# Optimization experiments

Hardware: AMD Instinct MI355X
Metric: run time of the kernel (lower is better)

## Reference

```python
import jax, jax.numpy as jnp
import numpy as np

BETA = 0.25  # commitment loss weight


def setup_inputs() -> dict:
    key = jax.random.key(0)
    ks = jax.random.split(key, 6)
    B, H, W, C = 16, 64, 64, 128
    x = jax.random.normal(ks[0], (B, H, W, C), dtype=jnp.float32)
    # dictionaries: sizes 2^6 .. 2^9 (from num_embeddings=[64,512]),
    # keras RandomUniform default init in (-0.05, 0.05)
    dicts = {}
    for i, n_emb in enumerate([64, 128, 256, 512]):
        dicts[f"dict{i}"] = jax.random.uniform(
            ks[i + 1], (C, n_emb), dtype=jnp.float32, minval=-0.05, maxval=0.05)
    vq_alpha = jnp.asarray(1.0, dtype=jnp.float32)
    vq_gamma = jnp.full((4,), 0.25, dtype=jnp.float32)  # 1/num_dictionaries
    return {"x": x, **dicts, "vq_alpha": vq_alpha, "vq_gamma": vq_gamma}


def _vq_pass(flat, D):
    # flat: [N, C], D: [C, K]. Squared-euclidean distances then argmin.
    dist = (jnp.sum(flat * flat, axis=1, keepdims=True)
            + jnp.sum(D * D, axis=0)[None, :]
            - 2.0 * (flat @ D))  # [N, K]
    idx = jnp.argmin(dist, axis=1)  # [N]
    # one_hot @ D.T  ==  gather rows of D.T
    return jnp.take(D.T, idx, axis=0)  # [N, C]


def reference(x, dict0, dict1, dict2, dict3, vq_alpha, vq_gamma):
    dicts = [dict0, dict1, dict2, dict3]
    C = x.shape[-1]
    flat = x.reshape(-1, C)  # [N, C]
    weighted_q = jnp.zeros_like(x)
    dictionary_loss = jnp.asarray(0.0, x.dtype)
    commitment_loss = jnp.asarray(0.0, x.dtype)
    for i, D in enumerate(dicts):
        q = (vq_alpha * _vq_pass(flat, D)).reshape(x.shape)
        weighted_q = weighted_q + vq_gamma[i] * q
        dictionary_loss += vq_gamma[i] * jnp.mean(
            jnp.square(jax.lax.stop_gradient(x) - q))
        commitment_loss += vq_gamma[i] * jnp.mean(
            jnp.square(x - jax.lax.stop_gradient(q)))
    loss = dictionary_loss + BETA * commitment_loss
    # straight-through estimator
    out = x + jax.lax.stop_gradient(weighted_q - x)
    return out, loss
```

## Files before the change

kernel.cpp:

```cpp
#include <hip/hip_runtime.h>

#define CDIM 128
#define NC   8388608

typedef __attribute__((ext_vector_type(8)))  short bf8v;
typedef __attribute__((ext_vector_type(16))) float f32x16;


__device__ __forceinline__ void bsplit(float v, short& h, short& lo) {
  unsigned u = __float_as_uint(v);
  unsigned hb = (u + 0x7fffu + ((u >> 16) & 1u)) >> 16;
  float hf = __uint_as_float(hb << 16);
  float lf = v - hf;
  unsigned u2 = __float_as_uint(lf);
  unsigned lb = (u2 + 0x7fffu + ((u2 >> 16) & 1u)) >> 16;
  h = (short)hb; lo = (short)lb;
}

__global__ void vq_prep(const float* __restrict__ D0, const float* __restrict__ D1,
                        const float* __restrict__ D2, const float* __restrict__ D3,
                        float* __restrict__ nrm, float* __restrict__ DT,
                        bf8v* __restrict__ Bph, bf8v* __restrict__ Bpl) {
  const int b = blockIdx.x;
  if (b < 60) {
    int g = b * 256 + threadIdx.x;
    int T = g >> 9, c = (g >> 6) & 7, l = g & 63;
    int col = T * 32 + (l & 31);
    int k0 = c * 16 + (l >> 5) * 8;
    const float* D; int K, cb;
    if (col < 64)       { D = D0; K = 64;  cb = col; }
    else if (col < 192) { D = D1; K = 128; cb = col - 64; }
    else if (col < 448) { D = D2; K = 256; cb = col - 192; }
    else                { D = D3; K = 512; cb = col - 448; }
    short h0,h1,h2,h3,h4,h5,h6,h7, q0,q1,q2,q3,q4,q5,q6,q7;
    bsplit(D[(k0+0)*K + cb], h0, q0);
    bsplit(D[(k0+1)*K + cb], h1, q1);
    bsplit(D[(k0+2)*K + cb], h2, q2);
    bsplit(D[(k0+3)*K + cb], h3, q3);
    bsplit(D[(k0+4)*K + cb], h4, q4);
    bsplit(D[(k0+5)*K + cb], h5, q5);
    bsplit(D[(k0+6)*K + cb], h6, q6);
    bsplit(D[(k0+7)*K + cb], h7, q7);
    Bph[g] = (bf8v){h0,h1,h2,h3,h4,h5,h6,h7};
    Bpl[g] = (bf8v){q0,q1,q2,q3,q4,q5,q6,q7};
  } else {
    int g = (b - 60) * 256 + threadIdx.x;
    if (g >= 960) return;
    const float* D; int K, k; float* T;
    if (g < 64)       { D = D0; K = 64;  k = g;       T = DT; }
    else if (g < 192) { D = D1; K = 128; k = g - 64;  T = DT + 8192; }
    else if (g < 448) { D = D2; K = 256; k = g - 192; T = DT + 24576; }
    else              { D = D3; K = 512; k = g - 448; T = DT + 57344; }
    float s = 0.f;
    for (int c = 0; c < 128; ++c) { float v = D[c*K+k]; s = fmaf(v,v,s); T[k*128+c] = v; }
    nrm[g] = s;
  }
}

#define MK8(U0, U1, HD, LD) { \
  short h0,h1,h2,h3,h4,h5,h6,h7, q0,q1,q2,q3,q4,q5,q6,q7; \
  bsplit(U0.x,h0,q0); bsplit(U0.y,h1,q1); bsplit(U0.z,h2,q2); bsplit(U0.w,h3,q3); \
  bsplit(U1.x,h4,q4); bsplit(U1.y,h5,q5); bsplit(U1.z,h6,q6); bsplit(U1.w,h7,q7); \
  HD = (bf8v){h0,h1,h2,h3,h4,h5,h6,h7}; \
  LD = (bf8v){q0,q1,q2,q3,q4,q5,q6,q7}; }

#define MFMA32(AC, AF, BF) AC = __builtin_amdgcn_mfma_f32_32x32x16_bf16((AF), (BF), (AC), 0, 0, 0)

#define PF_T(TT) { \
  const bf8v* __restrict__ gh = Bph + (TT) * 512; \
  const bf8v* __restrict__ gl = Bpl + (TT) * 512; \
  pf0 = gh[t]; pf1 = gh[256 + t]; pf2 = gl[t]; pf3 = gl[256 + t]; }

#define STORE_T(BF) { \
  BL[BF][t] = pf0; BL[BF][256 + t] = pf1; BL[BF][512 + t] = pf2; BL[BF][768 + t] = pf3; }

#define COMPUTE_T(T, BF) { \
  f32x16 ae = zero16, ao = zero16; \
  _Pragma("unroll") \
  for (int cp = 0; cp < 4; ++cp) { \
    const int ce = 2*cp, co = 2*cp+1; \
    bf8v bhe = BL[BF][ce*64 + l]; bf8v bho = BL[BF][co*64 + l]; \
    bf8v ble = BL[BF][512 + ce*64 + l]; bf8v blo = BL[BF][512 + co*64 + l]; \
    MFMA32(ae, Ah[ce], bhe); MFMA32(ao, Ah[co], bho); \
    MFMA32(ae, Al[ce], bhe); MFMA32(ao, Al[co], bho); \
    MFMA32(ae, Ah[ce], ble); MFMA32(ao, Ah[co], blo); \
  } \
  f32x16 sv = ae + ao; \
  const float nv = nrm_g[(T)*32 + (l & 31)]; \
  const int colT = (T)*32 + (l & 31); \
  _Pragma("unroll") \
  for (int r = 0; r < 16; ++r) { \
    float c0 = fmaf(-2.f, sv[r], nv); \
    if (c0 < bc[r]) { bc[r] = c0; bk[r] = colT; } } }

#define ROUND_T(T) { \
  if ((T) < 29) { \
    STORE_T(((T) + 1) & 1); \
    const int TN = ((T) + 2 <= 29) ? (T) + 2 : 29; \
    PF_T(TN); \
  } \
  COMPUTE_T(T, (T) & 1) \
  __syncthreads(); }

#define FLUSH1(DICTID, BASE, GAM) { \
  _Pragma("unroll") \
  for (int r = 0; r < 16; ++r) { \
    float b0 = bc[r]; int K0 = bk[r]; \
    _Pragma("unroll") \
    for (int m = 1; m <= 16; m <<= 1) { \
      float pb = __shfl_xor(b0, m); int pk = __shfl_xor(K0, m); \
      if (pb < b0 || (pb == b0 && pk < K0)) { b0 = pb; K0 = pk; } } \
    if ((l & 31) == 0) { \
      const int ro = (r & 3) + 8 * (r >> 2) + 4 * hl; \
      keysL[DICTID][w * 32 + ro] = K0 - (BASE); \
      const float nst = nrm_g[K0]; \
       \
      lossacc = fmaf((GAM) * a, fmaf(am1, nst, b0), lossacc); } \
    bc[r] = 1e30f; bk[r] = 0; } }

__global__ __launch_bounds__(256, 2) void vq_mfma(
    const float* __restrict__ x,
    const bf8v* __restrict__ Bph, const bf8v* __restrict__ Bpl,
    const float* __restrict__ nrm_g, const float* __restrict__ DT,
    const float* __restrict__ alpha_p, const float* __restrict__ gamma_p,
    float* __restrict__ out, float* __restrict__ partials)
{
  __shared__ bf8v  BL[2][1024];
  __shared__ int   keysL[4][128];
  __shared__ float lossW[4];

  const int t = threadIdx.x;
  const int w = t >> 6, l = t & 63;
  const int hl = l >> 5;
  const int rowbase = blockIdx.x * 128 + w * 32;

  const float a  = alpha_p[0];
  const float am1 = a - 1.f;
  const float g0 = gamma_p[0], g1 = gamma_p[1], g2 = gamma_p[2], g3 = gamma_p[3];
  const float gsum = g0 + g1 + g2 + g3;

  bf8v Ah[8], Al[8];
  float xsqh = 0.f;
  {
    const float* __restrict__ xr = x + (size_t)(rowbase + (l & 31)) * CDIM + hl * 8;
    #pragma unroll
    for (int c = 0; c < 8; ++c) {
      float4 u0 = *(const float4*)(xr + c * 16);
      float4 u1 = *(const float4*)(xr + c * 16 + 4);
      xsqh = fmaf(u0.x,u0.x, xsqh); xsqh = fmaf(u0.y,u0.y, xsqh);
      xsqh = fmaf(u0.z,u0.z, xsqh); xsqh = fmaf(u0.w,u0.w, xsqh);
      xsqh = fmaf(u1.x,u1.x, xsqh); xsqh = fmaf(u1.y,u1.y, xsqh);
      xsqh = fmaf(u1.z,u1.z, xsqh); xsqh = fmaf(u1.w,u1.w, xsqh);
      MK8(u0, u1, Ah[c], Al[c])
    }
  }
  float xs_ = xsqh;
  #pragma unroll
  for (int m = 1; m <= 32; m <<= 1) xs_ += __shfl_xor(xs_, m);

  f32x16 zero16;
  #pragma unroll
  for (int i = 0; i < 16; ++i) zero16[i] = 0.f;

  float bc[16]; int bk[16];
  #pragma unroll
  for (int r = 0; r < 16; ++r) { bc[r] = 1e30f; bk[r] = 0; }
  float lossacc = 0.f;

  bf8v pf0, pf1, pf2, pf3;
  PF_T(0)
  STORE_T(0)
  PF_T(1)
  __syncthreads();

  ROUND_T(0) ROUND_T(1)
  FLUSH1(0, 0, g0)
  for (int T = 2; T < 6; ++T) ROUND_T(T)
  FLUSH1(1, 64, g1)
  for (int T = 6; T < 14; ++T) ROUND_T(T)
  FLUSH1(2, 192, g2)
  for (int T = 14; T < 30; ++T) ROUND_T(T)
  FLUSH1(3, 448, g3)

  {
    float wl = lossacc + __shfl_xor(lossacc, 32);
    if (l == 0) lossW[w] = fmaf(gsum, xs_, wl);
  }
  __syncthreads();
  if (t == 0) partials[blockIdx.x] = lossW[0] + lossW[1] + lossW[2] + lossW[3];

  #pragma unroll 4
  for (int j = 0; j < 16; ++j) {
    const int f = j * 256 + t;
    const int r = f >> 5, c4 = (f & 31) * 4;
    const int kk0 = keysL[0][r], kk1 = keysL[1][r];
    const int kk2 = keysL[2][r], kk3 = keysL[3][r];
    const size_t off = (size_t)(blockIdx.x * 128 + r) * CDIM + c4;
    const float4 d0 = *(const float4*)(DT +         kk0 * 128 + c4);
    const float4 d1 = *(const float4*)(DT +  8192 + kk1 * 128 + c4);
    const float4 d2 = *(const float4*)(DT + 24576 + kk2 * 128 + c4);
    const float4 d3 = *(const float4*)(DT + 57344 + kk3 * 128 + c4);
    float4 o;
    o.x = a * (g0*d0.x + g1*d1.x + g2*d2.x + g3*d3.x);
    o.y = a * (g0*d0.y + g1*d1.y + g2*d2.y + g3*d3.y);
    o.z = a * (g0*d0.z + g1*d1.z + g2*d2.z + g3*d3.z);
    o.w = a * (g0*d0.w + g1*d1.w + g2*d2.w + g3*d3.w);
    *(float4*)(out + off) = o;
  }
}

__global__ void vq_loss(const float* __restrict__ partials, float* __restrict__ lossp) {
  __shared__ float wr[4];
  const int t = threadIdx.x;
  float v = partials[t] + partials[t + 256];
  #pragma unroll
  for (int off = 32; off > 0; off >>= 1) v += __shfl_down(v, off);
  if ((t & 63) == 0) wr[t >> 6] = v;
  __syncthreads();
  if (t == 0) lossp[0] = (wr[0] + wr[1] + wr[2] + wr[3]) * (1.25f / 8388608.f);
}

extern "C" void kernel_launch(void* const* d_in, const int* in_sizes, int n_in,
                              void* d_out, int out_size, void* d_ws, size_t ws_size,
                              hipStream_t stream) {
  const float* x  = (const float*)d_in[0];
  const float* D0 = (const float*)d_in[1];
  const float* D1 = (const float*)d_in[2];
  const float* D2 = (const float*)d_in[3];
  const float* D3 = (const float*)d_in[4];
  const float* alpha = (const float*)d_in[5];
  const float* gamma = (const float*)d_in[6];
  float* out = (float*)d_out;

  float* ws  = (float*)d_ws;
  float* nrm = ws;
  float* DT  = ws + 1024;
  bf8v*  Bph = (bf8v*)(ws + 123904);
  bf8v*  Bpl = (bf8v*)(ws + 185344);
  float* partials = ws + 246784;

  vq_prep<<<64, 256, 0, stream>>>(D0, D1, D2, D3, nrm, DT, Bph, Bpl);
  vq_mfma<<<512, 256, 0, stream>>>(x, Bph, Bpl, nrm, DT, alpha, gamma, out, partials);
  vq_loss<<<1, 256, 0, stream>>>(partials, out + NC);
}
```

Before: 104.2 us.

## Split codebook tiles across wave pairs and move gather-output into separate kernel

Each block now handles 64 rows instead of 128. Two waves scan dictionaries 0-2 (14 tiles) while the other two scan dictionary 3 (16 tiles) in parallel on the same rows, which halves the serial tile chain per wave. The grid doubles to 1024 blocks and occupancy is raised to 4 blocks per CU. Argmin keys go to a global buffer, and a new vq_merge kernel gathers and writes the weighted output. In exchange there is an extra launch and a key round-trip through memory, the prefetch-through-registers pipelining is replaced by synchronous staging with two barriers per round, and the part-0 waves sit idle for the last two rounds.

```diff
diff --git a/kernel.cpp b/kernel.cpp
--- a/kernel.cpp
+++ b/kernel.cpp
@@ -66,43 +66,38 @@
 
 #define MFMA32(AC, AF, BF) AC = __builtin_amdgcn_mfma_f32_32x32x16_bf16((AF), (BF), (AC), 0, 0, 0)
 
-#define PF_T(TT) { \
-  const bf8v* __restrict__ gh = Bph + (TT) * 512; \
-  const bf8v* __restrict__ gl = Bpl + (TT) * 512; \
-  pf0 = gh[t]; pf1 = gh[256 + t]; pf2 = gl[t]; pf3 = gl[256 + t]; }
-
-#define STORE_T(BF) { \
-  BL[BF][t] = pf0; BL[BF][256 + t] = pf1; BL[BF][512 + t] = pf2; BL[BF][768 + t] = pf3; }
-
-#define COMPUTE_T(T, BF) { \
+#define STAGE17(TP0, TP1, DO0) { \
+  if (DO0) { \
+    BL[0][t]       = Bph[(TP0) * 512 + t]; \
+    BL[0][256 + t] = Bph[(TP0) * 512 + 256 + t]; \
+    BL[0][512 + t] = Bpl[(TP0) * 512 + t]; \
+    BL[0][768 + t] = Bpl[(TP0) * 512 + 256 + t]; \
+  } \
+  BL[1][t]       = Bph[(TP1) * 512 + t]; \
+  BL[1][256 + t] = Bph[(TP1) * 512 + 256 + t]; \
+  BL[1][512 + t] = Bpl[(TP1) * 512 + t]; \
+  BL[1][768 + t] = Bpl[(TP1) * 512 + 256 + t]; }
+
+#define COMPUTE17(TT) { \
   f32x16 ae = zero16, ao = zero16; \
   _Pragma("unroll") \
   for (int cp = 0; cp < 4; ++cp) { \
     const int ce = 2*cp, co = 2*cp+1; \
-    bf8v bhe = BL[BF][ce*64 + l]; bf8v bho = BL[BF][co*64 + l]; \
-    bf8v ble = BL[BF][512 + ce*64 + l]; bf8v blo = BL[BF][512 + co*64 + l]; \
+    bf8v bhe = BL[part][ce*64 + l]; bf8v bho = BL[part][co*64 + l]; \
+    bf8v ble = BL[part][512 + ce*64 + l]; bf8v blo = BL[part][512 + co*64 + l]; \
     MFMA32(ae, Ah[ce], bhe); MFMA32(ao, Ah[co], bho); \
     MFMA32(ae, Al[ce], bhe); MFMA32(ao, Al[co], bho); \
     MFMA32(ae, Ah[ce], ble); MFMA32(ao, Ah[co], blo); \
   } \
   f32x16 sv = ae + ao; \
-  const float nv = nrm_g[(T)*32 + (l & 31)]; \
-  const int colT = (T)*32 + (l & 31); \
+  const float nv = nrm_g[(TT)*32 + (l & 31)]; \
+  const int colT = (TT)*32 + (l & 31); \
   _Pragma("unroll") \
   for (int r = 0; r < 16; ++r) { \
     float c0 = fmaf(-2.f, sv[r], nv); \
     if (c0 < bc[r]) { bc[r] = c0; bk[r] = colT; } } }
 
-#define ROUND_T(T) { \
-  if ((T) < 29) { \
-    STORE_T(((T) + 1) & 1); \
-    const int TN = ((T) + 2 <= 29) ? (T) + 2 : 29; \
-    PF_T(TN); \
-  } \
-  COMPUTE_T(T, (T) & 1) \
-  __syncthreads(); }
-
-#define FLUSH1(DICTID, BASE, GAM) { \
+#define FLUSH17(DICTID, BASE, GAM) { \
   _Pragma("unroll") \
   for (int r = 0; r < 16; ++r) { \
     float b0 = bc[r]; int K0 = bk[r]; \
@@ -112,29 +107,29 @@
       if (pb < b0 || (pb == b0 && pk < K0)) { b0 = pb; K0 = pk; } } \
     if ((l & 31) == 0) { \
       const int ro = (r & 3) + 8 * (r >> 2) + 4 * hl; \
-      keysL[DICTID][w * 32 + ro] = K0 - (BASE); \
+      keys[((rowbase + ro) << 2) | (DICTID)] = K0 - (BASE); \
       const float nst = nrm_g[K0]; \
-       \
       lossacc = fmaf((GAM) * a, fmaf(am1, nst, b0), lossacc); } \
     bc[r] = 1e30f; bk[r] = 0; } }
 
-__global__ __launch_bounds__(256, 2) void vq_mfma(
+__global__ __launch_bounds__(256, 4) void vq_mfma(
     const float* __restrict__ x,
     const bf8v* __restrict__ Bph, const bf8v* __restrict__ Bpl,
-    const float* __restrict__ nrm_g, const float* __restrict__ DT,
+    const float* __restrict__ nrm_g,
     const float* __restrict__ alpha_p, const float* __restrict__ gamma_p,
-    float* __restrict__ out, float* __restrict__ partials)
+    int* __restrict__ keys, float* __restrict__ partials)
 {
   __shared__ bf8v  BL[2][1024];
-  __shared__ int   keysL[4][128];
   __shared__ float lossW[4];
 
   const int t = threadIdx.x;
   const int w = t >> 6, l = t & 63;
   const int hl = l >> 5;
-  const int rowbase = blockIdx.x * 128 + w * 32;
-
-  const float a  = alpha_p[0];
+  const int rowt = w & 1;
+  const int part = w >> 1;
+  const int rowbase = blockIdx.x * 64 + rowt * 32;
+
+  const float a   = alpha_p[0];
   const float am1 = a - 1.f;
   const float g0 = gamma_p[0], g1 = gamma_p[1], g2 = gamma_p[2], g3 = gamma_p[3];
   const float gsum = g0 + g1 + g2 + g3;
@@ -167,39 +162,55 @@
   for (int r = 0; r < 16; ++r) { bc[r] = 1e30f; bk[r] = 0; }
   float lossacc = 0.f;
 
-  bf8v pf0, pf1, pf2, pf3;
-  PF_T(0)
-  STORE_T(0)
-  PF_T(1)
-  __syncthreads();
-
-  ROUND_T(0) ROUND_T(1)
-  FLUSH1(0, 0, g0)
-  for (int T = 2; T < 6; ++T) ROUND_T(T)
-  FLUSH1(1, 64, g1)
-  for (int T = 6; T < 14; ++T) ROUND_T(T)
-  FLUSH1(2, 192, g2)
-  for (int T = 14; T < 30; ++T) ROUND_T(T)
-  FLUSH1(3, 448, g3)
+  STAGE17(0, 14, true)
+  __syncthreads();
+
+  #pragma unroll 1
+  for (int r16i = 0; r16i < 16; ++r16i) {
+    if (part == 1) { COMPUTE17(14 + r16i) }
+    else if (r16i < 14) { COMPUTE17(r16i) }
+    if (part == 0) {
+      if (r16i == 1)       FLUSH17(0,   0, g0)
+      else if (r16i == 5)  FLUSH17(1,  64, g1)
+      else if (r16i == 13) FLUSH17(2, 192, g2)
+    } else if (r16i == 15) FLUSH17(3, 448, g3)
+    __syncthreads();
+    if (r16i < 15) {
+      const int n0 = (r16i + 1 < 14) ? r16i + 1 : 13;
+      STAGE17(n0, 15 + r16i, (r16i + 1 < 14))
+      __syncthreads();
+    }
+  }
 
   {
     float wl = lossacc + __shfl_xor(lossacc, 32);
-    if (l == 0) lossW[w] = fmaf(gsum, xs_, wl);
+    if (l == 0) lossW[w] = (part == 0) ? fmaf(gsum, xs_, wl) : wl;
   }
   __syncthreads();
   if (t == 0) partials[blockIdx.x] = lossW[0] + lossW[1] + lossW[2] + lossW[3];
-
-  #pragma unroll 4
-  for (int j = 0; j < 16; ++j) {
+}
+
+__global__ __launch_bounds__(256, 8) void vq_merge(
+    const float* __restrict__ DT, const int* __restrict__ keys,
+    const float* __restrict__ alpha_p, const float* __restrict__ gamma_p,
+    float* __restrict__ out)
+{
+  __shared__ int kk[32][4];
+  const int t = threadIdx.x;
+  const int row0 = blockIdx.x * 32;
+  if (t < 128) kk[t >> 2][t & 3] = keys[((row0 + (t >> 2)) << 2) | (t & 3)];
+  __syncthreads();
+  const float a = alpha_p[0];
+  const float g0 = gamma_p[0], g1 = gamma_p[1], g2 = gamma_p[2], g3 = gamma_p[3];
+  #pragma unroll
+  for (int j = 0; j < 4; ++j) {
     const int f = j * 256 + t;
     const int r = f >> 5, c4 = (f & 31) * 4;
-    const int kk0 = keysL[0][r], kk1 = keysL[1][r];
-    const int kk2 = keysL[2][r], kk3 = keysL[3][r];
-    const size_t off = (size_t)(blockIdx.x * 128 + r) * CDIM + c4;
-    const float4 d0 = *(const float4*)(DT +         kk0 * 128 + c4);
-    const float4 d1 = *(const float4*)(DT +  8192 + kk1 * 128 + c4);
-    const float4 d2 = *(const float4*)(DT + 24576 + kk2 * 128 + c4);
-    const float4 d3 = *(const float4*)(DT + 57344 + kk3 * 128 + c4);
+    const size_t off = (size_t)(row0 + r) * CDIM + c4;
+    const float4 d0 = *(const float4*)(DT +         kk[r][0] * 128 + c4);
+    const float4 d1 = *(const float4*)(DT +  8192 + kk[r][1] * 128 + c4);
+    const float4 d2 = *(const float4*)(DT + 24576 + kk[r][2] * 128 + c4);
+    const float4 d3 = *(const float4*)(DT + 57344 + kk[r][3] * 128 + c4);
     float4 o;
     o.x = a * (g0*d0.x + g1*d1.x + g2*d2.x + g3*d3.x);
     o.y = a * (g0*d0.y + g1*d1.y + g2*d2.y + g3*d3.y);
@@ -212,7 +223,7 @@
 __global__ void vq_loss(const float* __restrict__ partials, float* __restrict__ lossp) {
   __shared__ float wr[4];
   const int t = threadIdx.x;
-  float v = partials[t] + partials[t + 256];
+  float v = partials[t] + partials[t + 256] + partials[t + 512] + partials[t + 768];
   #pragma unroll
   for (int off = 32; off > 0; off >>= 1) v += __shfl_down(v, off);
   if ((t & 63) == 0) wr[t >> 6] = v;
@@ -237,9 +248,11 @@
   float* DT  = ws + 1024;
   bf8v*  Bph = (bf8v*)(ws + 123904);
   bf8v*  Bpl = (bf8v*)(ws + 185344);
-  float* partials = ws + 246784;
+  int*  keys = (int*)(ws + 246784);
+  float* partials = ws + 508928;
 
   vq_prep<<<64, 256, 0, stream>>>(D0, D1, D2, D3, nrm, DT, Bph, Bpl);
-  vq_mfma<<<512, 256, 0, stream>>>(x, Bph, Bpl, nrm, DT, alpha, gamma, out, partials);
+  vq_mfma<<<1024, 256, 0, stream>>>(x, Bph, Bpl, nrm, alpha, gamma, keys, partials);
+  vq_merge<<<2048, 256, 0, stream>>>(DT, keys, alpha, gamma, out);
   vq_loss<<<1, 256, 0, stream>>>(partials, out + NC);
 }
```

After: 204.8 us. +96.5%, slower.

## Split output gather into separate merge kernel via global key buffer

Applied to the files above, without the earlier changes.

Moves the final gather-and-weighted-sum of dictionary rows out of the MFMA distance kernel into a new vq_merge kernel with 2048 small blocks. The argmin indices are written to a global keys buffer instead of shared memory. The intent is to spread the memory-bound output write across many more blocks and free the compute kernel from the tail store phase. The cost is an extra kernel launch, a global round trip for the keys, and no overlap between the store and the MFMA work inside one block.

```diff
diff --git a/kernel.cpp b/kernel.cpp
--- a/kernel.cpp
+++ b/kernel.cpp
@@ -102,7 +102,7 @@
   COMPUTE_T(T, (T) & 1) \
   __syncthreads(); }
 
-#define FLUSH1(DICTID, BASE, GAM) { \
+#define FLUSHG(DICTID, BASE, GAM) { \
   _Pragma("unroll") \
   for (int r = 0; r < 16; ++r) { \
     float b0 = bc[r]; int K0 = bk[r]; \
@@ -112,7 +112,7 @@
       if (pb < b0 || (pb == b0 && pk < K0)) { b0 = pb; K0 = pk; } } \
     if ((l & 31) == 0) { \
       const int ro = (r & 3) + 8 * (r >> 2) + 4 * hl; \
-      keysL[DICTID][w * 32 + ro] = K0 - (BASE); \
+      keys[((rowbase + ro) << 2) | (DICTID)] = K0 - (BASE); \
       const float nst = nrm_g[K0]; \
        \
       lossacc = fmaf((GAM) * a, fmaf(am1, nst, b0), lossacc); } \
@@ -121,12 +121,11 @@
 __global__ __launch_bounds__(256, 2) void vq_mfma(
     const float* __restrict__ x,
     const bf8v* __restrict__ Bph, const bf8v* __restrict__ Bpl,
-    const float* __restrict__ nrm_g, const float* __restrict__ DT,
+    const float* __restrict__ nrm_g,
     const float* __restrict__ alpha_p, const float* __restrict__ gamma_p,
-    float* __restrict__ out, float* __restrict__ partials)
+    int* __restrict__ keys, float* __restrict__ partials)
 {
   __shared__ bf8v  BL[2][1024];
-  __shared__ int   keysL[4][128];
   __shared__ float lossW[4];
 
   const int t = threadIdx.x;
@@ -134,7 +133,7 @@
   const int hl = l >> 5;
   const int rowbase = blockIdx.x * 128 + w * 32;
 
-  const float a  = alpha_p[0];
+  const float a   = alpha_p[0];
   const float am1 = a - 1.f;
   const float g0 = gamma_p[0], g1 = gamma_p[1], g2 = gamma_p[2], g3 = gamma_p[3];
   const float gsum = g0 + g1 + g2 + g3;
@@ -174,13 +173,13 @@
   __syncthreads();
 
   ROUND_T(0) ROUND_T(1)
-  FLUSH1(0, 0, g0)
+  FLUSHG(0, 0, g0)
   for (int T = 2; T < 6; ++T) ROUND_T(T)
-  FLUSH1(1, 64, g1)
+  FLUSHG(1, 64, g1)
   for (int T = 6; T < 14; ++T) ROUND_T(T)
-  FLUSH1(2, 192, g2)
+  FLUSHG(2, 192, g2)
   for (int T = 14; T < 30; ++T) ROUND_T(T)
-  FLUSH1(3, 448, g3)
+  FLUSHG(3, 448, g3)
 
   {
     float wl = lossacc + __shfl_xor(lossacc, 32);
@@ -188,18 +187,29 @@
   }
   __syncthreads();
   if (t == 0) partials[blockIdx.x] = lossW[0] + lossW[1] + lossW[2] + lossW[3];
-
-  #pragma unroll 4
-  for (int j = 0; j < 16; ++j) {
+}
+
+__global__ __launch_bounds__(256, 8) void vq_merge(
+    const float* __restrict__ DT, const int* __restrict__ keys,
+    const float* __restrict__ alpha_p, const float* __restrict__ gamma_p,
+    float* __restrict__ out)
+{
+  __shared__ int kk[32][4];
+  const int t = threadIdx.x;
+  const int row0 = blockIdx.x * 32;
+  if (t < 128) kk[t >> 2][t & 3] = keys[((row0 + (t >> 2)) << 2) | (t & 3)];
+  __syncthreads();
+  const float a = alpha_p[0];
+  const float g0 = gamma_p[0], g1 = gamma_p[1], g2 = gamma_p[2], g3 = gamma_p[3];
+  #pragma unroll
+  for (int j = 0; j < 4; ++j) {
     const int f = j * 256 + t;
     const int r = f >> 5, c4 = (f & 31) * 4;
-    const int kk0 = keysL[0][r], kk1 = keysL[1][r];
-    const int kk2 = keysL[2][r], kk3 = keysL[3][r];
-    const size_t off = (size_t)(blockIdx.x * 128 + r) * CDIM + c4;
-    const float4 d0 = *(const float4*)(DT +         kk0 * 128 + c4);
-    const float4 d1 = *(const float4*)(DT +  8192 + kk1 * 128 + c4);
-    const float4 d2 = *(const float4*)(DT + 24576 + kk2 * 128 + c4);
-    const float4 d3 = *(const float4*)(DT + 57344 + kk3 * 128 + c4);
+    const size_t off = (size_t)(row0 + r) * CDIM + c4;
+    const float4 d0 = *(const float4*)(DT +         kk[r][0] * 128 + c4);
+    const float4 d1 = *(const float4*)(DT +  8192 + kk[r][1] * 128 + c4);
+    const float4 d2 = *(const float4*)(DT + 24576 + kk[r][2] * 128 + c4);
+    const float4 d3 = *(const float4*)(DT + 57344 + kk[r][3] * 128 + c4);
     float4 o;
     o.x = a * (g0*d0.x + g1*d1.x + g2*d2.x + g3*d3.x);
     o.y = a * (g0*d0.y + g1*d1.y + g2*d2.y + g3*d3.y);
@@ -237,9 +247,11 @@
   float* DT  = ws + 1024;
   bf8v*  Bph = (bf8v*)(ws + 123904);
   bf8v*  Bpl = (bf8v*)(ws + 185344);
-  float* partials = ws + 246784;
+  int*  keys = (int*)(ws + 246784);
+  float* partials = ws + 508928;
 
   vq_prep<<<64, 256, 0, stream>>>(D0, D1, D2, D3, nrm, DT, Bph, Bpl);
-  vq_mfma<<<512, 256, 0, stream>>>(x, Bph, Bpl, nrm, DT, alpha, gamma, out, partials);
+  vq_mfma<<<512, 256, 0, stream>>>(x, Bph, Bpl, nrm, alpha, gamma, keys, partials);
+  vq_merge<<<2048, 256, 0, stream>>>(DT, keys, alpha, gamma, out);
   vq_loss<<<1, 256, 0, stream>>>(partials, out + NC);
 }
```

New measurement: 99.56 us (median of 3 runs). 1.05x faster.
